# Kernel optimization log

Hardware: AMD Instinct MI355X
Metric: run time of the kernel (lower is better)

## Reference

```python
import jax, jax.numpy as jnp
import numpy as np

B, N, D, A = 2048, 32, 64, 8
MAX_ACTION = 1.0
VARIANCE = 1.0


def setup_inputs() -> dict:
    key = jax.random.key(0)
    k1, k2, k3, k4, k5 = jax.random.split(key, 5)
    mean = jax.random.normal(k1, (B, D), dtype=jnp.float32)
    # SPD covariance: small-scale L L^T + 0.1 I
    L = jax.random.normal(k2, (B, D, D), dtype=jnp.float32) * 0.05
    covariance = jnp.einsum('bij,bkj->bik', L, L) + 0.1 * jnp.eye(D, dtype=jnp.float32)
    centers = jax.random.normal(k3, (N, D), dtype=jnp.float32) * 0.5
    weights = jax.random.normal(k4, (N, A), dtype=jnp.float32) * 0.1
    lengthscales = jnp.ones((D,), dtype=jnp.float32) + 0.1 * jax.random.uniform(k5, (D,), dtype=jnp.float32)
    return {"mean": mean, "covariance": covariance, "centers": centers,
            "weights": weights, "lengthscales": lengthscales}


def squash_sin(mean, covariance, max_action):
    # mean: (B, K); covariance: (B, K, K)
    K = mean.shape[-1]
    ma = jnp.full((K,), max_action, dtype=mean.dtype)
    diag_cov = jnp.diagonal(covariance, axis1=-2, axis2=-1)          # (B, K)
    squashed_mean = ma * jnp.exp(-diag_cov / 2.0) * jnp.sin(mean)
    lq = -(diag_cov[..., :, None] + diag_cov[..., None, :]) / 2.0
    q = jnp.exp(lq)
    mean_diff = mean[..., :, None] - mean[..., None, :]
    mean_sum = mean[..., :, None] + mean[..., None, :]
    sq_cov = ((jnp.exp(lq + covariance) - q) * jnp.cos(mean_diff)
              - (jnp.exp(lq - covariance) - q) * jnp.cos(mean_sum))
    outer_max = ma[None, :] * ma[:, None]
    sq_cov = outer_max * sq_cov / 2.0
    # diag_embed of (B, K) -> (B, K, K)
    cross = (ma * jnp.exp(-diag_cov / 2.0) * jnp.cos(mean))[..., :, None] * jnp.eye(K, dtype=mean.dtype)
    return squashed_mean, sq_cov, cross


def reference(mean, covariance, centers, weights, lengthscales):
    b = mean.shape[0]
    inv_l = 1.0 / lengthscales                                        # (D,)
    # B_mat = diag(inv_l) @ cov @ diag(inv_l) + I  (B, D, D)
    B_mat = covariance * (inv_l[:, None] * inv_l[None, :]) + jnp.eye(D, dtype=mean.dtype)
    inp = centers[None, :, :] - mean[:, None, :]                      # (B, N, D)
    scaled_inp = inp * inv_l                                          # (B, N, D)
    t = jnp.swapaxes(jnp.linalg.solve(B_mat, jnp.swapaxes(scaled_inp, -1, -2)), -1, -2)  # (B, N, D)
    exp_term = jnp.exp(-0.5 * jnp.sum(scaled_inp * t, axis=-1))       # (B, N)
    _, log_det = jnp.linalg.slogdet(B_mat)                            # (B,)
    normalizer = VARIANCE * jnp.exp(-0.5 * log_det)
    phi_mean = normalizer[:, None] * exp_term                         # (B, N)
    action_mean = phi_mean @ weights                                  # (B, A)

    t_scaled = t * inv_l                                              # (B, N, D)
    cross_cov = jnp.einsum('bnd,bna->bda', t_scaled, phi_mean[..., None] * weights)  # (B, D, A)

    diff = centers[:, None, :] - centers[None, :, :]                  # (N, N, D)
    center_bar = (centers[:, None, :] + centers[None, :, :]) / 2.0    # (N, N, D)
    inv_lambda = 1.0 / lengthscales ** 2
    exp1 = -0.25 * jnp.sum(diff ** 2 * inv_lambda, axis=-1)           # (N, N)
    B_q = covariance + jnp.diag(lengthscales ** 2 / 2.0)[None]        # (B, D, D)
    z = center_bar[None] - mean[:, None, None, :]                     # (B, N, N, D)
    z_flat = z.reshape(b, N * N, D)
    solved = jnp.swapaxes(jnp.linalg.solve(B_q, jnp.swapaxes(z_flat, -1, -2)), -1, -2)
    exp2 = (-0.5 * jnp.sum(z_flat * solved, axis=-1)).reshape(b, N, N)
    log_det_lh = jnp.sum(jnp.log(lengthscales ** 2 / 2.0))
    _, log_det_bq = jnp.linalg.slogdet(B_q)
    c_q = jnp.exp(0.5 * (log_det_lh - log_det_bq))                    # (B,)
    Q = (VARIANCE ** 2) * c_q[:, None, None] * jnp.exp(exp1[None] + exp2)  # (B, N, N)

    action_cov = jnp.einsum('na,bnm,mc->bac', weights, Q, weights)    # (B, A, A)
    action_cov = action_cov - action_mean[:, :, None] * action_mean[:, None, :]
    action_cov = (action_cov + jnp.swapaxes(action_cov, -1, -2)) / 2.0
    action_cov = action_cov + jnp.eye(A, dtype=mean.dtype) * 1e-6

    action_mean, action_cov, C = squash_sin(action_mean, action_cov, MAX_ACTION)
    cross_cov = jnp.einsum('bda,bac->bdc', cross_cov, C)
    return (action_mean, action_cov, cross_cov)
```

## Files before the change

kernel.cpp:

```cpp
#include <hip/hip_runtime.h>
#include <math.h>


#define DD 64
#define NN 32
#define AA 8
#define NBATCH 2048
#define STR 68
#define W9 9

__global__ void rbf_prep(const float* __restrict__ centers,
                         const float* __restrict__ ls,
                         float* __restrict__ ws) {
    __shared__ float cen_s[NN * DD];
    __shared__ float il2_s[DD];
    int t = threadIdx.x;
    for (int e = t; e < NN * DD; e += 256) cen_s[e] = centers[e];
    if (t < DD) { float l = ls[t]; il2_s[t] = 1.0f / (l * l); }
    __syncthreads();
    int p = blockIdx.x * 256 + t;
    if (p < NN * NN) {
        int n = p >> 5, m = p & 31;
        float acc = 0.f;
        for (int d = 0; d < DD; ++d) {
            float df = cen_s[n * DD + d] - cen_s[m * DD + d];
            acc += df * df * il2_s[d];
        }
        ws[p] = -0.25f * acc;
    }
    if (blockIdx.x == 0 && t < DD) {
        float l = ls[t];
        float v = logf(0.5f * l * l);
        #pragma unroll
        for (int o = 1; o < 64; o <<= 1) v += __shfl_xor(v, o, 64);
        if (t == 0) ws[NN * NN] = v;
    }
}

__device__ __forceinline__ void factor_panel(float (&A)[4][4], const int p,
    float* __restrict__ LmT, float* __restrict__ diag_s, float* __restrict__ invd_s,
    const int lw)
{
    const int rb  = lw & 15;
    const int cbl = lw >> 4;
    const int c0  = 16 * p + 4 * cbl;
    const int r0  = 4 * rb;
    #pragma unroll
    for (int jj = 0; jj < 16; ++jj) {
        const int q  = jj >> 2;
        const int ci = jj & 3;
        const int j  = 16 * p + jj;
        const int fsrc = rb | (q << 4);
        const int hsrc = (4 * p + cbl) | (q << 4);
        const int dsrc = (4 * p + q) | (q << 4);
        float d  = __shfl(A[ci][ci], dsrc, 64);
        float f0 = __shfl(A[0][ci], fsrc, 64);
        float f1 = __shfl(A[1][ci], fsrc, 64);
        float f2 = __shfl(A[2][ci], fsrc, 64);
        float f3 = __shfl(A[3][ci], fsrc, 64);
        float h0 = __shfl(A[0][ci], hsrc, 64);
        float h1 = __shfl(A[1][ci], hsrc, 64);
        float h2 = __shfl(A[2][ci], hsrc, 64);
        float h3 = __shfl(A[3][ci], hsrc, 64);
        float id = __builtin_amdgcn_rcpf(d);
        float fr[4];
        fr[0] = (r0 + 0 > j) ? f0 : 0.f;
        fr[1] = (r0 + 1 > j) ? f1 : 0.f;
        fr[2] = (r0 + 2 > j) ? f2 : 0.f;
        fr[3] = (r0 + 3 > j) ? f3 : 0.f;
        float hc[4];
        hc[0] = (c0 + 0 > j) ? h0 * id : 0.f;
        hc[1] = (c0 + 1 > j) ? h1 * id : 0.f;
        hc[2] = (c0 + 2 > j) ? h2 * id : 0.f;
        hc[3] = (c0 + 3 > j) ? h3 * id : 0.f;
        #pragma unroll
        for (int s = 0; s < 4; ++s)
            #pragma unroll
            for (int c = 0; c < 4; ++c)
                A[s][c] -= fr[s] * hc[c];
        if (cbl == 0) {
            float4 v = make_float4(fr[0] * id, fr[1] * id, fr[2] * id, fr[3] * id);
            *(float4*)&LmT[j * STR + r0] = v;
        }
        if (lw == jj) { diag_s[j] = d; invd_s[j] = id; }
    }
}

__device__ __forceinline__ void trailing_one(float (&A)[4][4], const int p,
    const float* __restrict__ LmT, const float* __restrict__ diag_s,
    const int rb, const int cbX)
{
    #pragma unroll 2
    for (int kk = 0; kk < 16; ++kk) {
        const int k = 16 * p + kk;
        const float4 Lr = *(const float4*)&LmT[k * STR + 4 * rb];
        const float4 Lc = *(const float4*)&LmT[k * STR + 4 * cbX];
        const float dk = diag_s[k];
        const float h0 = Lc.x * dk, h1 = Lc.y * dk, h2 = Lc.z * dk, h3 = Lc.w * dk;
        A[0][0] -= Lr.x * h0; A[0][1] -= Lr.x * h1; A[0][2] -= Lr.x * h2; A[0][3] -= Lr.x * h3;
        A[1][0] -= Lr.y * h0; A[1][1] -= Lr.y * h1; A[1][2] -= Lr.y * h2; A[1][3] -= Lr.y * h3;
        A[2][0] -= Lr.z * h0; A[2][1] -= Lr.z * h1; A[2][2] -= Lr.z * h2; A[2][3] -= Lr.z * h3;
        A[3][0] -= Lr.w * h0; A[3][1] -= Lr.w * h1; A[3][2] -= Lr.w * h2; A[3][3] -= Lr.w * h3;
    }
}

__global__ __launch_bounds__(256, 3) void rbf_main(
    const float* __restrict__ mean,
    const float* __restrict__ cov,
    const float* __restrict__ centers,
    const float* __restrict__ weights,
    const float* __restrict__ ls,
    const float* __restrict__ ws,
    float* __restrict__ out)
{
    __shared__ __align__(16) float LmT1[DD * STR];
    __shared__ __align__(16) float U2s[DD * STR];
    __shared__ __align__(16) float phiwc[NN * AA];
    __shared__ float diag1[DD], invd1[DD], diag2[DD], invd2[DD];
    __shared__ float mean_s[DD], invl_s[DD], l2h_s[DD];
    __shared__ float w9_s[NN * W9], U_s[NN * W9];
    __shared__ float am_s[AA], acr_s[AA * W9], Ca_s[AA];
    __shared__ float ldlh_s;

    float* const LmT2 = U2s;
    float* const H_s  = U2s;
    float* const K_s  = U2s + NN * STR;
    float* const cp_s = U2s + NN * STR + DD * W9;

    const int t   = threadIdx.x;
    const int b   = blockIdx.x;
    const int lw  = t & 63;
    const int wv  = t >> 6;
    const int rb  = t & 15;
    const int cb  = t >> 4;
    const int cb1 = (cb + 8) & 15;
    const int wp1 = (wv + 2) & 3;
    const int l8  = t & 7;
    const float* cvb = cov + (size_t)b * DD * DD;

    if (t < DD) {
        float l = ls[t];
        invl_s[t] = 1.0f / l;
        l2h_s[t]  = 0.5f * l * l;
        mean_s[t] = mean[(size_t)b * DD + t];
    }
    w9_s[(t >> 3) * W9 + (t & 7)] = weights[t];
    if (t == 0) ldlh_s = ws[NN * NN];
    __syncthreads();

    float A1[4][4], A2[4][4];
    {
        #pragma unroll
        for (int c = 0; c < 4; ++c) {
            const int gr = 4 * cb + c;
            const float4 cv = *(const float4*)(cvb + (size_t)gr * DD + 4 * rb);
            A2[0][c] = cv.x + ((4*rb+0 == gr) ? l2h_s[gr] : 0.0f);
            A2[1][c] = cv.y + ((4*rb+1 == gr) ? l2h_s[gr] : 0.0f);
            A2[2][c] = cv.z + ((4*rb+2 == gr) ? l2h_s[gr] : 0.0f);
            A2[3][c] = cv.w + ((4*rb+3 == gr) ? l2h_s[gr] : 0.0f);
        }
        const float il0 = invl_s[4*rb+0], il1 = invl_s[4*rb+1],
                    il2 = invl_s[4*rb+2], il3 = invl_s[4*rb+3];
        #pragma unroll
        for (int c = 0; c < 4; ++c) {
            const int gr = 4 * cb1 + c;
            const float4 cv = *(const float4*)(cvb + (size_t)gr * DD + 4 * rb);
            const float ilc = invl_s[gr];
            A1[0][c] = cv.x * il0 * ilc + ((4*rb+0 == gr) ? 1.0f : 0.0f);
            A1[1][c] = cv.y * il1 * ilc + ((4*rb+1 == gr) ? 1.0f : 0.0f);
            A1[2][c] = cv.z * il2 * ilc + ((4*rb+2 == gr) ? 1.0f : 0.0f);
            A1[3][c] = cv.w * il3 * ilc + ((4*rb+3 == gr) ? 1.0f : 0.0f);
        }
    }

    if (wv == 0) factor_panel(A2, 0, LmT2, diag2, invd2, lw);
    if (wv == 2) factor_panel(A1, 0, LmT1, diag1, invd1, lw);
    #pragma unroll 1
    for (int p = 0; p < 3; ++p) {
        __syncthreads();
        if (wv  >= p + 1) trailing_one(A2, p, LmT2, diag2, rb, cb);
        if (wp1 >= p + 1) trailing_one(A1, p, LmT1, diag1, rb, cb1);
        if (wv == p + 1)         factor_panel(A2, p + 1, LmT2, diag2, invd2, lw);
        if (wv == ((p + 3) & 3)) factor_panel(A1, p + 1, LmT1, diag1, invd1, lw);
    }
    __syncthreads();

    float logdet1, cq;
    {
        float v1 = logf(diag1[lw]);
        float v2 = logf(diag2[lw]);
        #pragma unroll
        for (int o = 1; o < 64; o <<= 1) {
            v1 += __shfl_xor(v1, o, 64);
            v2 += __shfl_xor(v2, o, 64);
        }
        logdet1 = v1;
        cq = expf(0.5f * (ldlh_s - v2));
    }

    if (wv == 0) {
        const int gr8 = lw >> 3;
        float x0[8], x1v[8], x2v[8], x3v[8];
        #pragma unroll
        for (int rr = 0; rr < 4; ++rr) {
            const int n = gr8 + 8 * rr;
            const float4 ca = *(const float4*)(centers + n * DD + 8 * l8);
            const float4 cz = *(const float4*)(centers + n * DD + 8 * l8 + 4);
            float da[8] = {ca.x,ca.y,ca.z,ca.w,cz.x,cz.y,cz.z,cz.w};
            float* xp = (rr == 0) ? x0 : (rr == 1) ? x1v : (rr == 2) ? x2v : x3v;
            #pragma unroll
            for (int s = 0; s < 8; ++s) {
                const int i = 8 * l8 + s;
                xp[s] = (da[s] - mean_s[i]) * invl_s[i];
            }
        }
        for (int k8 = 0; k8 < 8; ++k8) {
            #pragma unroll
            for (int kk = 0; kk < 8; ++kk) {
                const int k = 8 * k8 + kk;
                const int src = (lw & 56) | k8;
                float z0 = __shfl(x0[kk],  src, 64);
                float z1 = __shfl(x1v[kk], src, 64);
                float z2 = __shfl(x2v[kk], src, 64);
                float z3 = __shfl(x3v[kk], src, 64);
                const float4 LA = *(const float4*)&LmT1[k * STR + 8 * l8];
                const float4 LB = *(const float4*)&LmT1[k * STR + 8 * l8 + 4];
                float l1[8] = {LA.x,LA.y,LA.z,LA.w,LB.x,LB.y,LB.z,LB.w};
                #pragma unroll
                for (int s = 0; s < 8; ++s) {
                    x0[s]  -= l1[s] * z0;
                    x1v[s] -= l1[s] * z1;
                    x2v[s] -= l1[s] * z2;
                    x3v[s] -= l1[s] * z3;
                }
            }
        }
        #pragma unroll
        for (int rr = 0; rr < 4; ++rr) {
            const int n = gr8 + 8 * rr;
            const float* xp = (rr == 0) ? x0 : (rr == 1) ? x1v : (rr == 2) ? x2v : x3v;
            float qf = 0.f;
            #pragma unroll
            for (int s = 0; s < 8; ++s) qf += xp[s] * xp[s] * invd1[8 * l8 + s];
            qf += __shfl_xor(qf, 1, 64);
            qf += __shfl_xor(qf, 2, 64);
            qf += __shfl_xor(qf, 4, 64);
            float ph = expf(-0.5f * (logdet1 + qf));
            phiwc[n * AA + l8] = ph * w9_s[n * W9 + l8];
        }
    } else if (wv == 1) {
        const int gr8 = lw >> 3;
        float x0[8], x1v[8], x2v[8], x3v[8];
        #pragma unroll
        for (int rr = 0; rr < 4; ++rr) {
            const int n = gr8 + 8 * rr;
            const float4 ca = *(const float4*)(centers + n * DD + 8 * l8);
            const float4 cz = *(const float4*)(centers + n * DD + 8 * l8 + 4);
            float da[8] = {ca.x,ca.y,ca.z,ca.w,cz.x,cz.y,cz.z,cz.w};
            float* xp = (rr == 0) ? x0 : (rr == 1) ? x1v : (rr == 2) ? x2v : x3v;
            #pragma unroll
            for (int s = 0; s < 8; ++s) {
                const int i = 8 * l8 + s;
                xp[s] = 0.5f * (da[s] - mean_s[i]);
            }
        }
        for (int k8 = 0; k8 < 8; ++k8) {
            #pragma unroll
            for (int kk = 0; kk < 8; ++kk) {
                const int k = 8 * k8 + kk;
                const int src = (lw & 56) | k8;
                float z0 = __shfl(x0[kk],  src, 64);
                float z1 = __shfl(x1v[kk], src, 64);
                float z2 = __shfl(x2v[kk], src, 64);
                float z3 = __shfl(x3v[kk], src, 64);
                const float4 MA = *(const float4*)&LmT2[k * STR + 8 * l8];
                const float4 MB = *(const float4*)&LmT2[k * STR + 8 * l8 + 4];
                float l2[8] = {MA.x,MA.y,MA.z,MA.w,MB.x,MB.y,MB.z,MB.w};
                #pragma unroll
                for (int s = 0; s < 8; ++s) {
                    x0[s]  -= l2[s] * z0;
                    x1v[s] -= l2[s] * z1;
                    x2v[s] -= l2[s] * z2;
                    x3v[s] -= l2[s] * z3;
                }
            }
        }
        #pragma unroll
        for (int rr = 0; rr < 4; ++rr) {
            const int n = gr8 + 8 * rr;
            const float* xp = (rr == 0) ? x0 : (rr == 1) ? x1v : (rr == 2) ? x2v : x3v;
            float h[8];
            #pragma unroll
            for (int s = 0; s < 8; ++s) h[s] = xp[s] * sqrtf(invd2[8 * l8 + s]);
            *(float4*)&H_s[n * STR + 8 * l8]     = make_float4(h[0],h[1],h[2],h[3]);
            *(float4*)&H_s[n * STR + 8 * l8 + 4] = make_float4(h[4],h[5],h[6],h[7]);
        }
    }
    __syncthreads();

    if (wv == 0) {
        {
            const int d = lw;
            const float md = mean_s[d], il = invl_s[d];
            float k0=0.f,k1=0.f,k2=0.f,k3=0.f,k4=0.f,k5=0.f,k6=0.f,k7=0.f;
            for (int n = 0; n < NN; ++n) {
                const float sv = (centers[n * DD + d] - md) * il;
                const float4 pa = *(const float4*)&phiwc[n * AA];
                const float4 pb = *(const float4*)&phiwc[n * AA + 4];
                k0 += sv * pa.x; k1 += sv * pa.y; k2 += sv * pa.z; k3 += sv * pa.w;
                k4 += sv * pb.x; k5 += sv * pb.y; k6 += sv * pb.z; k7 += sv * pb.w;
            }
            K_s[d*W9+0]=k0; K_s[d*W9+1]=k1; K_s[d*W9+2]=k2; K_s[d*W9+3]=k3;
            K_s[d*W9+4]=k4; K_s[d*W9+5]=k5; K_s[d*W9+6]=k6; K_s[d*W9+7]=k7;
        }
        const int aa = lw >> 3;
        float y[8];
        #pragma unroll
        for (int s = 0; s < 8; ++s) y[s] = K_s[(8 * l8 + s) * W9 + aa];
        for (int k8 = 0; k8 < 8; ++k8) {
            #pragma unroll
            for (int kk = 0; kk < 8; ++kk) {
                const int k = 8 * k8 + kk;
                float zk = __shfl(y[kk], (lw & 56) | k8, 64);
                const float4 f0 = *(const float4*)&LmT1[k * STR + 8 * l8];
                const float4 f1 = *(const float4*)&LmT1[k * STR + 8 * l8 + 4];
                y[0] -= f0.x * zk; y[1] -= f0.y * zk;
                y[2] -= f0.z * zk; y[3] -= f0.w * zk;
                y[4] -= f1.x * zk; y[5] -= f1.y * zk;
                y[6] -= f1.z * zk; y[7] -= f1.w * zk;
            }
        }
        #pragma unroll
        for (int s = 0; s < 8; ++s) y[s] *= invd1[8 * l8 + s];
        for (int i8 = 7; i8 >= 0; --i8) {
            #pragma unroll
            for (int ii = 7; ii >= 0; --ii) {
                const int i = 8 * i8 + ii;
                const float4 r0 = *(const float4*)&LmT1[i * STR + 8 * l8];
                const float4 r1 = *(const float4*)&LmT1[i * STR + 8 * l8 + 4];
                float part = r0.x*y[0] + r0.y*y[1] + r0.z*y[2] + r0.w*y[3]
                           + r1.x*y[4] + r1.y*y[5] + r1.z*y[6] + r1.w*y[7];
                part += __shfl_xor(part, 1, 64);
                part += __shfl_xor(part, 2, 64);
                part += __shfl_xor(part, 4, 64);
                if (l8 == i8) y[ii] -= part;
            }
        }
        #pragma unroll
        for (int s = 0; s < 8; ++s)
            cp_s[(8 * l8 + s) * W9 + aa] = y[s] * invl_s[8 * l8 + s];
    } else if (wv == 3) {
        if (lw < AA) {
            const int a = lw;
            float am = 0.f;
            for (int n = 0; n < NN; ++n) am += phiwc[n * AA + a];
            am_s[a] = am;
        }
    } else {
        const int g16 = (lw >> 3) + 8 * (wv - 1);
        const int n0 = g16, n1 = g16 + 16;
        float acc0[4] = {0.f,0.f,0.f,0.f}, acc1[4] = {0.f,0.f,0.f,0.f};
        const int rot = 2 * l8;
        #pragma unroll 2
        for (int e = 0; e < 16; ++e) {
            const int e4 = 4 * ((e + rot) & 15);
            const float4 hn0 = *(const float4*)&H_s[n0 * STR + e4];
            const float4 hn1 = *(const float4*)&H_s[n1 * STR + e4];
            #pragma unroll
            for (int mm = 0; mm < 4; ++mm) {
                const float4 hm = *(const float4*)&H_s[(4 * l8 + mm) * STR + e4];
                {
                    float s0 = hn0.x + hm.x, s1 = hn0.y + hm.y;
                    float s2 = hn0.z + hm.z, s3 = hn0.w + hm.w;
                    acc0[mm] += s0*s0 + s1*s1 + s2*s2 + s3*s3;
                }
                {
                    float s0 = hn1.x + hm.x, s1 = hn1.y + hm.y;
                    float s2 = hn1.z + hm.z, s3 = hn1.w + hm.w;
                    acc1[mm] += s0*s0 + s1*s1 + s2*s2 + s3*s3;
                }
            }
        }
        const float4 e1a = *(const float4*)&ws[n0 * NN + 4 * l8];
        const float4 e1b = *(const float4*)&ws[n1 * NN + 4 * l8];
        float Q0a = cq * expf(e1a.x - 0.5f * acc0[0]);
        float Q1a = cq * expf(e1a.y - 0.5f * acc0[1]);
        float Q2a = cq * expf(e1a.z - 0.5f * acc0[2]);
        float Q3a = cq * expf(e1a.w - 0.5f * acc0[3]);
        float Q0b = cq * expf(e1b.x - 0.5f * acc1[0]);
        float Q1b = cq * expf(e1b.y - 0.5f * acc1[1]);
        float Q2b = cq * expf(e1b.z - 0.5f * acc1[2]);
        float Q3b = cq * expf(e1b.w - 0.5f * acc1[3]);
        float ua[8], ub[8];
        #pragma unroll
        for (int a = 0; a < 8; ++a) {
            const float w0 = w9_s[(4*l8+0)*W9 + a], w1 = w9_s[(4*l8+1)*W9 + a];
            const float w2 = w9_s[(4*l8+2)*W9 + a], w3 = w9_s[(4*l8+3)*W9 + a];
            ua[a] = Q0a*w0 + Q1a*w1 + Q2a*w2 + Q3a*w3;
            ub[a] = Q0b*w0 + Q1b*w1 + Q2b*w2 + Q3b*w3;
            ua[a] += __shfl_xor(ua[a], 1, 64);
            ua[a] += __shfl_xor(ua[a], 2, 64);
            ua[a] += __shfl_xor(ua[a], 4, 64);
            ub[a] += __shfl_xor(ub[a], 1, 64);
            ub[a] += __shfl_xor(ub[a], 2, 64);
            ub[a] += __shfl_xor(ub[a], 4, 64);
        }
        float uva = (l8 == 0) ? ua[0] : (l8 == 1) ? ua[1] : (l8 == 2) ? ua[2] : (l8 == 3) ? ua[3]
                  : (l8 == 4) ? ua[4] : (l8 == 5) ? ua[5] : (l8 == 6) ? ua[6] : ua[7];
        float uvb = (l8 == 0) ? ub[0] : (l8 == 1) ? ub[1] : (l8 == 2) ? ub[2] : (l8 == 3) ? ub[3]
                  : (l8 == 4) ? ub[4] : (l8 == 5) ? ub[5] : (l8 == 6) ? ub[6] : ub[7];
        U_s[n0 * W9 + l8] = uva;
        U_s[n1 * W9 + l8] = uvb;
    }
    __syncthreads();

    if (t < 64) {
        const int a = t >> 3, c = t & 7;
        float acc2 = 0.f;
        for (int n = 0; n < NN; ++n) acc2 += w9_s[n * W9 + a] * U_s[n * W9 + c];
        acr_s[a * W9 + c] = acc2;
    }
    __syncthreads();

    float* out0 = out;
    float* out1 = out + (size_t)NBATCH * AA;
    float* out2 = out + (size_t)NBATCH * AA + (size_t)NBATCH * AA * AA;
    if (t < 64) {
        const int a = t >> 3, c = t & 7;
        const float ama = am_s[a], amc = am_s[c];
        const float vac = 0.5f * (acr_s[a * W9 + c] + acr_s[c * W9 + a])
                        - ama * amc + ((a == c) ? 1e-6f : 0.0f);
        const float dca = acr_s[a * W9 + a] - ama * ama + 1e-6f;
        const float dcc = acr_s[c * W9 + c] - amc * amc + 1e-6f;
        const float q = expf(-0.5f * (dca + dcc));
        const float sq = 0.5f * q * (expm1f(vac) * cosf(ama - amc)
                                   - expm1f(-vac) * cosf(ama + amc));
        out1[(size_t)b * 64 + t] = sq;
        if (t < AA) {
            float dct = acr_s[t * W9 + t] - am_s[t] * am_s[t] + 1e-6f;
            float e = expf(-0.5f * dct);
            out0[(size_t)b * AA + t] = e * sinf(am_s[t]);
            Ca_s[t] = e * cosf(am_s[t]);
        }
    }
    __syncthreads();
    #pragma unroll
    for (int e = 0; e < 2; ++e) {
        int idx = t + 256 * e;
        out2[(size_t)b * 512 + idx] = cp_s[(idx >> 3) * W9 + (idx & 7)] * Ca_s[idx & 7];
    }
}

extern "C" void kernel_launch(void* const* d_in, const int* in_sizes, int n_in,
                              void* d_out, int out_size, void* d_ws, size_t ws_size,
                              hipStream_t stream) {
    (void)in_sizes; (void)n_in; (void)out_size; (void)ws_size;
    const float* mean    = (const float*)d_in[0];
    const float* cov     = (const float*)d_in[1];
    const float* centers = (const float*)d_in[2];
    const float* weights = (const float*)d_in[3];
    const float* ls      = (const float*)d_in[4];
    float* ws = (float*)d_ws;
    float* o  = (float*)d_out;
    rbf_prep<<<4, 256, 0, stream>>>(centers, ls, ws);
    rbf_main<<<NBATCH, 256, 0, stream>>>(mean, cov, centers, weights, ls, ws, o);
}
```

Before: 212.7 us.

## Replace blocked 4x4 LDL factorization with per-wave row-per-lane readlane factorization

Swaps the cooperative blocked LDL^T factorization, which spreads 4x4 register tiles across all four waves with shuffles and block barriers between panels, for a scheme where one wave factors each 64x64 matrix. Each lane holds one full row in 64 registers and broadcasts pivots and pivot-row entries with readlane, so the inter-panel __syncthreads are gone. The costs are heavy register use (launch bounds lowered from 3 to 2 blocks per CU), two of four waves idling during the factorization, and a long serial dependency chain of scalar readlanes.

```diff
diff --git a/kernel.cpp b/kernel.cpp
--- a/kernel.cpp
+++ b/kernel.cpp
@@ -8,6 +8,10 @@
 #define NBATCH 2048
 #define STR 68
 #define W9 9
+
+__device__ __forceinline__ float frl(float v, int lane) {
+    return __int_as_float(__builtin_amdgcn_readlane(__float_as_int(v), lane));
+}
 
 __global__ void rbf_prep(const float* __restrict__ centers,
                          const float* __restrict__ ls,
@@ -37,74 +41,7 @@
     }
 }
 
-__device__ __forceinline__ void factor_panel(float (&A)[4][4], const int p,
-    float* __restrict__ LmT, float* __restrict__ diag_s, float* __restrict__ invd_s,
-    const int lw)
-{
-    const int rb  = lw & 15;
-    const int cbl = lw >> 4;
-    const int c0  = 16 * p + 4 * cbl;
-    const int r0  = 4 * rb;
-    #pragma unroll
-    for (int jj = 0; jj < 16; ++jj) {
-        const int q  = jj >> 2;
-        const int ci = jj & 3;
-        const int j  = 16 * p + jj;
-        const int fsrc = rb | (q << 4);
-        const int hsrc = (4 * p + cbl) | (q << 4);
-        const int dsrc = (4 * p + q) | (q << 4);
-        float d  = __shfl(A[ci][ci], dsrc, 64);
-        float f0 = __shfl(A[0][ci], fsrc, 64);
-        float f1 = __shfl(A[1][ci], fsrc, 64);
-        float f2 = __shfl(A[2][ci], fsrc, 64);
-        float f3 = __shfl(A[3][ci], fsrc, 64);
-        float h0 = __shfl(A[0][ci], hsrc, 64);
-        float h1 = __shfl(A[1][ci], hsrc, 64);
-        float h2 = __shfl(A[2][ci], hsrc, 64);
-        float h3 = __shfl(A[3][ci], hsrc, 64);
-        float id = __builtin_amdgcn_rcpf(d);
-        float fr[4];
-        fr[0] = (r0 + 0 > j) ? f0 : 0.f;
-        fr[1] = (r0 + 1 > j) ? f1 : 0.f;
-        fr[2] = (r0 + 2 > j) ? f2 : 0.f;
-        fr[3] = (r0 + 3 > j) ? f3 : 0.f;
-        float hc[4];
-        hc[0] = (c0 + 0 > j) ? h0 * id : 0.f;
-        hc[1] = (c0 + 1 > j) ? h1 * id : 0.f;
-        hc[2] = (c0 + 2 > j) ? h2 * id : 0.f;
-        hc[3] = (c0 + 3 > j) ? h3 * id : 0.f;
-        #pragma unroll
-        for (int s = 0; s < 4; ++s)
-            #pragma unroll
-            for (int c = 0; c < 4; ++c)
-                A[s][c] -= fr[s] * hc[c];
-        if (cbl == 0) {
-            float4 v = make_float4(fr[0] * id, fr[1] * id, fr[2] * id, fr[3] * id);
-            *(float4*)&LmT[j * STR + r0] = v;
-        }
-        if (lw == jj) { diag_s[j] = d; invd_s[j] = id; }
-    }
-}
-
-__device__ __forceinline__ void trailing_one(float (&A)[4][4], const int p,
-    const float* __restrict__ LmT, const float* __restrict__ diag_s,
-    const int rb, const int cbX)
-{
-    #pragma unroll 2
-    for (int kk = 0; kk < 16; ++kk) {
-        const int k = 16 * p + kk;
-        const float4 Lr = *(const float4*)&LmT[k * STR + 4 * rb];
-        const float4 Lc = *(const float4*)&LmT[k * STR + 4 * cbX];
-        const float dk = diag_s[k];
-        const float h0 = Lc.x * dk, h1 = Lc.y * dk, h2 = Lc.z * dk, h3 = Lc.w * dk;
-        A[0][0] -= Lr.x * h0; A[0][1] -= Lr.x * h1; A[0][2] -= Lr.x * h2; A[0][3] -= Lr.x * h3;
-        A[1][0] -= Lr.y * h0; A[1][1] -= Lr.y * h1; A[1][2] -= Lr.y * h2; A[1][3] -= Lr.y * h3;
-        A[2][0] -= Lr.z * h0; A[2][1] -= Lr.z * h1; A[2][2] -= Lr.z * h2; A[2][3] -= Lr.z * h3;
-        A[3][0] -= Lr.w * h0; A[3][1] -= Lr.w * h1; A[3][2] -= Lr.w * h2; A[3][3] -= Lr.w * h3;
-    }
-}
-
-__global__ __launch_bounds__(256, 3) void rbf_main(
+__global__ __launch_bounds__(256, 2) void rbf_main(
     const float* __restrict__ mean,
     const float* __restrict__ cov,
     const float* __restrict__ centers,
@@ -131,10 +68,6 @@
     const int b   = blockIdx.x;
     const int lw  = t & 63;
     const int wv  = t >> 6;
-    const int rb  = t & 15;
-    const int cb  = t >> 4;
-    const int cb1 = (cb + 8) & 15;
-    const int wp1 = (wv + 2) & 3;
     const int l8  = t & 7;
     const float* cvb = cov + (size_t)b * DD * DD;
 
@@ -148,40 +81,54 @@
     if (t == 0) ldlh_s = ws[NN * NN];
     __syncthreads();
 
-    float A1[4][4], A2[4][4];
-    {
-        #pragma unroll
-        for (int c = 0; c < 4; ++c) {
-            const int gr = 4 * cb + c;
-            const float4 cv = *(const float4*)(cvb + (size_t)gr * DD + 4 * rb);
-            A2[0][c] = cv.x + ((4*rb+0 == gr) ? l2h_s[gr] : 0.0f);
-            A2[1][c] = cv.y + ((4*rb+1 == gr) ? l2h_s[gr] : 0.0f);
-            A2[2][c] = cv.z + ((4*rb+2 == gr) ? l2h_s[gr] : 0.0f);
-            A2[3][c] = cv.w + ((4*rb+3 == gr) ? l2h_s[gr] : 0.0f);
-        }
-        const float il0 = invl_s[4*rb+0], il1 = invl_s[4*rb+1],
-                    il2 = invl_s[4*rb+2], il3 = invl_s[4*rb+3];
-        #pragma unroll
-        for (int c = 0; c < 4; ++c) {
-            const int gr = 4 * cb1 + c;
-            const float4 cv = *(const float4*)(cvb + (size_t)gr * DD + 4 * rb);
-            const float ilc = invl_s[gr];
-            A1[0][c] = cv.x * il0 * ilc + ((4*rb+0 == gr) ? 1.0f : 0.0f);
-            A1[1][c] = cv.y * il1 * ilc + ((4*rb+1 == gr) ? 1.0f : 0.0f);
-            A1[2][c] = cv.z * il2 * ilc + ((4*rb+2 == gr) ? 1.0f : 0.0f);
-            A1[3][c] = cv.w * il3 * ilc + ((4*rb+3 == gr) ? 1.0f : 0.0f);
-        }
-    }
-
-    if (wv == 0) factor_panel(A2, 0, LmT2, diag2, invd2, lw);
-    if (wv == 2) factor_panel(A1, 0, LmT1, diag1, invd1, lw);
-    #pragma unroll 1
-    for (int p = 0; p < 3; ++p) {
-        __syncthreads();
-        if (wv  >= p + 1) trailing_one(A2, p, LmT2, diag2, rb, cb);
-        if (wp1 >= p + 1) trailing_one(A1, p, LmT1, diag1, rb, cb1);
-        if (wv == p + 1)         factor_panel(A2, p + 1, LmT2, diag2, invd2, lw);
-        if (wv == ((p + 3) & 3)) factor_panel(A1, p + 1, LmT1, diag1, invd1, lw);
+    if ((wv & 1) == 0 && wv < 4) {
+        float Ar[DD];
+        const float ilr  = invl_s[lw];
+        const float l2hr = l2h_s[lw];
+        const float* rowp = cvb + (size_t)lw * DD;
+        if (wv == 0) {
+            #pragma unroll
+            for (int c4 = 0; c4 < DD / 4; ++c4) {
+                const float4 cv = *(const float4*)(rowp + 4 * c4);
+                float v0 = (cv.x * ilr) * frl(ilr, 4*c4+0);
+                float v1 = (cv.y * ilr) * frl(ilr, 4*c4+1);
+                float v2 = (cv.z * ilr) * frl(ilr, 4*c4+2);
+                float v3 = (cv.w * ilr) * frl(ilr, 4*c4+3);
+                if (lw == 4*c4+0) v0 += 1.0f;
+                if (lw == 4*c4+1) v1 += 1.0f;
+                if (lw == 4*c4+2) v2 += 1.0f;
+                if (lw == 4*c4+3) v3 += 1.0f;
+                Ar[4*c4+0] = v0; Ar[4*c4+1] = v1;
+                Ar[4*c4+2] = v2; Ar[4*c4+3] = v3;
+            }
+        } else {
+            #pragma unroll
+            for (int c4 = 0; c4 < DD / 4; ++c4) {
+                const float4 cv = *(const float4*)(rowp + 4 * c4);
+                float v0 = cv.x, v1 = cv.y, v2 = cv.z, v3 = cv.w;
+                if (lw == 4*c4+0) v0 += l2hr;
+                if (lw == 4*c4+1) v1 += l2hr;
+                if (lw == 4*c4+2) v2 += l2hr;
+                if (lw == 4*c4+3) v3 += l2hr;
+                Ar[4*c4+0] = v0; Ar[4*c4+1] = v1;
+                Ar[4*c4+2] = v2; Ar[4*c4+3] = v3;
+            }
+        }
+        float* const Lp = (wv == 0) ? LmT1 : LmT2;
+        float dreg = 0.0f, ireg = 0.0f;
+        #pragma unroll
+        for (int j = 0; j < DD; ++j) {
+            const float dj = frl(Ar[j], j);
+            const float id = __builtin_amdgcn_rcpf(dj);
+            const float g  = (lw > j) ? Ar[j] * id : 0.0f;
+            Lp[j * STR + lw] = g;
+            if (lw == j) { dreg = dj; ireg = id; }
+            #pragma unroll
+            for (int c = j + 1; c < DD; ++c)
+                Ar[c] -= g * frl(Ar[j], c);
+        }
+        if (wv == 0) { diag1[lw] = dreg; invd1[lw] = ireg; }
+        else         { diag2[lw] = dreg; invd2[lw] = ireg; }
     }
     __syncthreads();
 
```

New measurement: 227.6 us. 1.07x slower.
